# Kernel optimization log

Measured on AMD Instinct MI355X. Metric: run time of the kernel, lower is better.

The kernel has to match this reference:

```python
import jax, jax.numpy as jnp
import numpy as np

N_NODES = 50000
N_EDGES = 1_000_000
N_HYPER = 1024
F_IN = 128
F_EDGE = 64


def setup_inputs() -> dict:
    key = jax.random.key(0)
    ks = jax.random.split(key, 20)
    s = 0.05
    return {
        "x": jax.random.normal(ks[0], (N_NODES, F_IN), jnp.float32),
        "edge_index": jax.random.randint(ks[1], (2, N_EDGES), 0, N_NODES, dtype=jnp.int64),
        "edge_weight": jax.random.uniform(ks[2], (N_EDGES,), jnp.float32),
        "edge_features": jax.random.normal(ks[3], (N_HYPER, F_EDGE), jnp.float32),
        "adj_e": jax.random.uniform(ks[4], (N_HYPER, N_HYPER), jnp.float32) / N_HYPER,
        "T": jax.random.uniform(ks[5], (N_NODES, N_HYPER), jnp.float32) / N_HYPER,
        # HypergraphConvLayer 1: 128 -> 64
        "W1": jax.random.normal(ks[6], (F_IN, 64), jnp.float32) * s,
        "b1": jnp.zeros((64,), jnp.float32),
        # HypergraphConvLayer 2: 64 -> 32
        "W2": jax.random.normal(ks[7], (64, 32), jnp.float32) * s,
        "b2": jnp.zeros((32,), jnp.float32),
        # GraphConvolution (CensNet-style): node 32->32, edge 64->32
        "Wn": jax.random.normal(ks[8], (32, 32), jnp.float32) * s,
        "We": jax.random.normal(ks[9], (F_EDGE, 32), jnp.float32) * s,
        "bg": jnp.zeros((32,), jnp.float32),
        # class_classifier: Linear(32,32) -> ReLU -> Linear(32,2) -> Softmax
        "Wc1": jax.random.normal(ks[10], (32, 32), jnp.float32) * s,
        "bc1": jnp.zeros((32,), jnp.float32),
        "Wc2": jax.random.normal(ks[11], (32, 2), jnp.float32) * s,
        "bc2": jnp.zeros((2,), jnp.float32),
    }


def _hconv(h, W, b, src, dst, edge_weight, num_nodes):
    # linear projection then edge-weighted scatter-add: out[dst] += w * h[src]
    h = h @ W + b
    msg = h[src] * edge_weight[:, None]          # [E, d]
    return jax.ops.segment_sum(msg, dst, num_segments=num_nodes)


def reference(x, edge_index, edge_weight, edge_features, adj_e, T,
              W1, b1, W2, b2, Wn, We, bg, Wc1, bc1, Wc2, bc2):
    n = x.shape[0]
    src, dst = edge_index[0], edge_index[1]

    h = jax.nn.relu(_hconv(x, W1, b1, src, dst, edge_weight, n))   # [N,64]
    h = jax.nn.relu(_hconv(h, W2, b2, src, dst, edge_weight, n))   # [N,32]

    # aggregate_node_features: node_features[dst] += h[src]; / num_edges
    num_edges = edge_index.shape[1]
    node_features = jax.ops.segment_sum(h[src], dst, num_segments=n) / num_edges

    # edge_conv: node linear + incidence-weighted hyperedge convolution
    edge_h = adj_e @ (edge_features @ We)                           # [NE,32]
    shared = jax.nn.relu(node_features @ Wn + T @ edge_h + bg)      # [N,32]

    # class_classifier
    c = jax.nn.relu(shared @ Wc1 + bc1)
    logits = c @ Wc2 + bc2
    return jax.nn.softmax(logits, axis=1)                           # [N,2]
```

## Files before the change

kernel.cpp:

```cpp
#include <hip/hip_runtime.h>
#include <hip/hip_bf16.h>

template<int COLS, int K, int RPBT>
__global__ __launch_bounds__(256) void gemm_k(
    const float* __restrict__ X, const float* __restrict__ W,
    const float* __restrict__ bias, float* __restrict__ out,
    int nrows, float scale, int relu_in)
{
    constexpr int CPT = COLS / 8;
    constexpr int KT  = 32;
    constexpr int NKT = K / KT;
    constexpr int RT  = RPBT / 32;

    __shared__ float sx[RPBT * 36];
    __shared__ float sWT[COLS * 33];

    const int tid = threadIdx.x;
    const int cg  = tid & 7;
    const int rg  = tid >> 3;
    const int r0  = blockIdx.x * RPBT;

    float acc[RT][CPT];
    #pragma unroll
    for (int r = 0; r < RT; ++r)
        #pragma unroll
        for (int c = 0; c < CPT; ++c) acc[r][c] = 0.f;

    for (int kt = 0; kt < NKT; ++kt) {
        #pragma unroll
        for (int j = 0; j < RT; ++j) {
            int i  = tid + j * 256;
            int r  = i >> 3;
            int k4 = i & 7;
            int gr = r0 + r; if (gr >= nrows) gr = nrows - 1;
            float4 v = *(const float4*)&X[(size_t)gr * K + kt * KT + k4 * 4];
            if (relu_in) {
                v.x = fmaxf(v.x, 0.f); v.y = fmaxf(v.y, 0.f);
                v.z = fmaxf(v.z, 0.f); v.w = fmaxf(v.w, 0.f);
            }
            if (scale != 1.f) { v.x *= scale; v.y *= scale; v.z *= scale; v.w *= scale; }
            *(float4*)&sx[r * 36 + k4 * 4] = v;
        }
        for (int i = tid; i < COLS * KT; i += 256) {
            int kl = i / COLS, c = i % COLS;
            sWT[c * 33 + kl] = W[(size_t)(kt * KT + kl) * COLS + c];
        }
        __syncthreads();

        #pragma unroll
        for (int k4 = 0; k4 < 8; ++k4) {
            float4 a[RT];
            #pragma unroll
            for (int r = 0; r < RT; ++r)
                a[r] = *(const float4*)&sx[(r * 32 + rg) * 36 + k4 * 4];
            #pragma unroll
            for (int cc = 0; cc < CPT; ++cc) {
                int c = cg * CPT + cc;
                float w0 = sWT[c * 33 + k4 * 4 + 0];
                float w1 = sWT[c * 33 + k4 * 4 + 1];
                float w2 = sWT[c * 33 + k4 * 4 + 2];
                float w3 = sWT[c * 33 + k4 * 4 + 3];
                #pragma unroll
                for (int r = 0; r < RT; ++r)
                    acc[r][cc] += a[r].x * w0 + a[r].y * w1 + a[r].z * w2 + a[r].w * w3;
            }
        }
        __syncthreads();
    }

    #pragma unroll
    for (int r = 0; r < RT; ++r) {
        int row = r0 + r * 32 + rg;
        if (row < nrows) {
            #pragma unroll
            for (int cc4 = 0; cc4 < CPT / 4; ++cc4) {
                int c = cg * CPT + cc4 * 4;
                float4 o;
                o.x = acc[r][cc4 * 4 + 0] + (bias ? bias[c + 0] : 0.f);
                o.y = acc[r][cc4 * 4 + 1] + (bias ? bias[c + 1] : 0.f);
                o.z = acc[r][cc4 * 4 + 2] + (bias ? bias[c + 2] : 0.f);
                o.w = acc[r][cc4 * 4 + 3] + (bias ? bias[c + 3] : 0.f);
                *(float4*)&out[(size_t)row * COLS + c] = o;
            }
        }
    }
}

__global__ __launch_bounds__(256, 4) void tgemm2_k(
    const float* __restrict__ T, const float* __restrict__ eh,
    float* __restrict__ par, int nrows)
{
    __shared__ float seh[256 * 32];
    const int tid = threadIdx.x;
    const int ks  = blockIdx.y * 256;

    #pragma unroll
    for (int j = 0; j < 8; ++j) {
        int i = tid + j * 256;
        *(float4*)&seh[i * 4] = *(const float4*)&eh[(size_t)ks * 32 + (size_t)i * 4];
    }
    __syncthreads();

    int row = blockIdx.x * 256 + tid;
    int r   = row < nrows ? row : nrows - 1;
    const float* Tp = T + (size_t)r * 1024 + ks;

    float acc[32];
    #pragma unroll
    for (int c = 0; c < 32; ++c) acc[c] = 0.f;

    float4 t[8];
    #pragma unroll
    for (int q = 0; q < 8; ++q) t[q] = *(const float4*)&Tp[q * 4];

    for (int kc = 0; kc < 8; ++kc) {
        float4 tn[8];
        if (kc < 7) {
            #pragma unroll
            for (int q = 0; q < 8; ++q)
                tn[q] = *(const float4*)&Tp[(kc + 1) * 32 + q * 4];
        }
        #pragma unroll
        for (int q = 0; q < 8; ++q) {
            #pragma unroll
            for (int j = 0; j < 4; ++j) {
                float a = (j == 0) ? t[q].x : (j == 1) ? t[q].y : (j == 2) ? t[q].z : t[q].w;
                int k = kc * 32 + q * 4 + j;
                #pragma unroll
                for (int c4 = 0; c4 < 8; ++c4) {
                    float4 w = *(const float4*)&seh[k * 32 + c4 * 4];
                    acc[c4 * 4 + 0] += a * w.x;
                    acc[c4 * 4 + 1] += a * w.y;
                    acc[c4 * 4 + 2] += a * w.z;
                    acc[c4 * 4 + 3] += a * w.w;
                }
            }
        }
        #pragma unroll
        for (int q = 0; q < 8; ++q) t[q] = tn[q];
    }

    if (row < nrows) {
        float* p = par + (size_t)blockIdx.y * nrows * 32 + (size_t)row * 32;
        #pragma unroll
        for (int c4 = 0; c4 < 8; ++c4)
            *(float4*)&p[c4 * 4] = make_float4(acc[c4 * 4 + 0], acc[c4 * 4 + 1],
                                               acc[c4 * 4 + 2], acc[c4 * 4 + 3]);
    }
}

__global__ __launch_bounds__(256) void classify_k(
    const float* __restrict__ par, const float* __restrict__ nfw,
    const float* __restrict__ bg, const float* __restrict__ Wc1,
    const float* __restrict__ bc1, const float* __restrict__ Wc2,
    const float* __restrict__ bc2, float* __restrict__ out, int nrows)
{
    __shared__ float sWc1T[1024];
    __shared__ float sWc2[64];
    __shared__ float sb[66];

    int tid = threadIdx.x;
    for (int i = tid; i < 1024; i += 256)
        sWc1T[(i & 31) * 32 + (i >> 5)] = Wc1[i];
    if (tid < 64) sWc2[tid] = Wc2[tid];
    if (tid < 32)      sb[tid] = bc1[tid];
    else if (tid < 64) sb[tid] = bg[tid - 32];
    else if (tid < 66) sb[tid] = bc2[tid - 64];
    __syncthreads();

    int row = blockIdx.x * 256 + tid;
    if (row >= nrows) return;

    size_t stride = (size_t)nrows * 32;
    float4 sh4[8];
    #pragma unroll
    for (int i4 = 0; i4 < 8; ++i4) {
        const float* base = par + (size_t)row * 32 + i4 * 4;
        float4 v0 = *(const float4*)(base);
        float4 v1 = *(const float4*)(base + stride);
        float4 v2 = *(const float4*)(base + 2 * stride);
        float4 v3 = *(const float4*)(base + 3 * stride);
        float4 nf = *(const float4*)&nfw[(size_t)row * 32 + i4 * 4];
        float4 o;
        o.x = fmaxf(v0.x + v1.x + v2.x + v3.x + nf.x + sb[32 + i4 * 4 + 0], 0.f);
        o.y = fmaxf(v0.y + v1.y + v2.y + v3.y + nf.y + sb[32 + i4 * 4 + 1], 0.f);
        o.z = fmaxf(v0.z + v1.z + v2.z + v3.z + nf.z + sb[32 + i4 * 4 + 2], 0.f);
        o.w = fmaxf(v0.w + v1.w + v2.w + v3.w + nf.w + sb[32 + i4 * 4 + 3], 0.f);
        sh4[i4] = o;
    }

    float l0 = sb[64], l1 = sb[65];
    #pragma unroll
    for (int jj = 0; jj < 32; ++jj) {
        float s = sb[jj];
        #pragma unroll
        for (int i4 = 0; i4 < 8; ++i4) {
            float4 w4 = *(const float4*)&sWc1T[jj * 32 + i4 * 4];
            s += sh4[i4].x * w4.x + sh4[i4].y * w4.y
               + sh4[i4].z * w4.z + sh4[i4].w * w4.w;
        }
        s = fmaxf(s, 0.f);
        l0 += s * sWc2[jj * 2 + 0];
        l1 += s * sWc2[jj * 2 + 1];
    }
    float p0 = 1.f / (1.f + expf(l1 - l0));
    float p1 = 1.f / (1.f + expf(l0 - l1));
    *(float2*)&out[(size_t)row * 2] = make_float2(p0, p1);
}

__global__ void hist_k(const int* __restrict__ dst, int* __restrict__ deg, int E)
{
    int e = blockIdx.x * 256 + threadIdx.x;
    if (e < E) atomicAdd(&deg[dst[e]], 1);
}

__global__ void scan1_k(const int* __restrict__ deg, int* __restrict__ bsum, int N)
{
    __shared__ int s[256];
    int t = threadIdx.x, i = blockIdx.x * 256 + t;
    s[t] = (i < N) ? deg[i] : 0;
    __syncthreads();
    for (int off = 128; off > 0; off >>= 1) {
        if (t < off) s[t] += s[t + off];
        __syncthreads();
    }
    if (t == 0) bsum[blockIdx.x] = s[0];
}

__global__ void scan2_k(const int* __restrict__ bsum, int* __restrict__ boff,
                        int NB, int* __restrict__ rsN)
{
    __shared__ int s[256];
    int t = threadIdx.x;
    int v = (t < NB) ? bsum[t] : 0;
    s[t] = v;
    __syncthreads();
    for (int off = 1; off < 256; off <<= 1) {
        int u = (t >= off) ? s[t - off] : 0;
        __syncthreads();
        s[t] += u;
        __syncthreads();
    }
    if (t < NB) boff[t] = s[t] - v;
    if (t == NB - 1) *rsN = s[t];
}

__global__ void scan3_k(const int* __restrict__ deg, const int* __restrict__ boff,
                        int* __restrict__ rs, int* __restrict__ cur, int N)
{
    __shared__ int s[256];
    int t = threadIdx.x, i = blockIdx.x * 256 + t;
    int v = (i < N) ? deg[i] : 0;
    s[t] = v;
    __syncthreads();
    for (int off = 1; off < 256; off <<= 1) {
        int u = (t >= off) ? s[t - off] : 0;
        __syncthreads();
        s[t] += u;
        __syncthreads();
    }
    if (i < N) {
        int ex = boff[blockIdx.x] + s[t] - v;
        rs[i] = ex;
        cur[i] = ex;
    }
}

__global__ void fill_k(const int* __restrict__ src, const int* __restrict__ dst,
                       const float* __restrict__ ew, int* __restrict__ cur,
                       int2* __restrict__ epk, int E)
{
    int e = blockIdx.x * 256 + threadIdx.x;
    if (e < E) {
        int pos = atomicAdd(&cur[dst[e]], 1);
        epk[pos] = make_int2(src[e], __float_as_int(ew[e]));
    }
}

__global__ __launch_bounds__(256) void gather64w_k(
    const float* __restrict__ hp, const int2* __restrict__ epk,
    const int* __restrict__ rs, float* __restrict__ outv, int N)
{
    int wid  = (blockIdx.x * 256 + threadIdx.x) >> 6;
    if (wid >= N) return;
    int lane = threadIdx.x & 63;
    int e4   = lane >> 4;
    int ch   = lane & 15;
    int j0 = rs[wid], j1 = rs[wid + 1];

    float4 acc = make_float4(0.f, 0.f, 0.f, 0.f);
    for (int j = j0 + e4; j < j1; j += 4) {
        int2 e = epk[j];
        float w = __int_as_float(e.y);
        float4 v = *(const float4*)&hp[(size_t)e.x * 64 + ch * 4];
        acc.x += v.x * w; acc.y += v.y * w;
        acc.z += v.z * w; acc.w += v.w * w;
    }
    #pragma unroll
    for (int off = 16; off < 64; off <<= 1) {
        acc.x += __shfl_xor(acc.x, off);
        acc.y += __shfl_xor(acc.y, off);
        acc.z += __shfl_xor(acc.z, off);
        acc.w += __shfl_xor(acc.w, off);
    }
    if (e4 == 0)
        *(float4*)&outv[(size_t)wid * 64 + ch * 4] = acc;
}

template<bool WEIGHTED, bool RELU>
__global__ __launch_bounds__(256) void gather32w_k(
    const float* __restrict__ hp, const int2* __restrict__ epk,
    const int* __restrict__ rs, float* __restrict__ outv, int N)
{
    int wid  = (blockIdx.x * 256 + threadIdx.x) >> 6;
    if (wid >= N) return;
    int lane = threadIdx.x & 63;
    int e8   = lane >> 3;
    int ch   = lane & 7;
    int j0 = rs[wid], j1 = rs[wid + 1];

    float4 acc = make_float4(0.f, 0.f, 0.f, 0.f);
    for (int j = j0 + e8; j < j1; j += 8) {
        int2 e = epk[j];
        float w = WEIGHTED ? __int_as_float(e.y) : 1.f;
        float4 v = *(const float4*)&hp[(size_t)e.x * 32 + ch * 4];
        if (RELU) {
            v.x = fmaxf(v.x, 0.f); v.y = fmaxf(v.y, 0.f);
            v.z = fmaxf(v.z, 0.f); v.w = fmaxf(v.w, 0.f);
        }
        acc.x += v.x * w; acc.y += v.y * w;
        acc.z += v.z * w; acc.w += v.w * w;
    }
    #pragma unroll
    for (int off = 8; off < 64; off <<= 1) {
        acc.x += __shfl_xor(acc.x, off);
        acc.y += __shfl_xor(acc.y, off);
        acc.z += __shfl_xor(acc.z, off);
        acc.w += __shfl_xor(acc.w, off);
    }
    if (e8 == 0)
        *(float4*)&outv[(size_t)wid * 32 + ch * 4] = acc;
}

__global__ void efwe_k(const float* __restrict__ ef, const float* __restrict__ We,
                       float* __restrict__ tmp)
{
    int idx = blockIdx.x * 256 + threadIdx.x;
    int row = idx >> 5, c = idx & 31;
    float s = 0.f;
    #pragma unroll
    for (int k = 0; k < 64; ++k)
        s += ef[row * 64 + k] * We[k * 32 + c];
    tmp[row * 32 + c] = s;
}

__global__ void adjmm_k(const float* __restrict__ adj, const float* __restrict__ tmp,
                        float* __restrict__ edge_h)
{
    int kq     = blockIdx.x & 3;
    int rowblk = blockIdx.x >> 2;
    int r = rowblk * 8 + (threadIdx.x >> 5);
    int c = threadIdx.x & 31;
    float s = 0.f;
    int k0 = kq * 256;
    #pragma unroll 8
    for (int k = k0; k < k0 + 256; ++k)
        s += adj[r * 1024 + k] * tmp[k * 32 + c];
    atomicAdd(&edge_h[r * 32 + c], s);
}

extern "C" void kernel_launch(void* const* d_in, const int* in_sizes, int n_in,
                              void* d_out, int out_size, void* d_ws, size_t ws_size,
                              hipStream_t stream)
{
    const float* x   = (const float*)d_in[0];
    const int*   ei  = (const int*)  d_in[1];
    const float* ew  = (const float*)d_in[2];
    const float* ef  = (const float*)d_in[3];
    const float* adj = (const float*)d_in[4];
    const float* T   = (const float*)d_in[5];
    const float* W1  = (const float*)d_in[6];
    const float* b1  = (const float*)d_in[7];
    const float* W2  = (const float*)d_in[8];
    const float* b2  = (const float*)d_in[9];
    const float* Wn  = (const float*)d_in[10];
    const float* We  = (const float*)d_in[11];
    const float* bg  = (const float*)d_in[12];
    const float* Wc1 = (const float*)d_in[13];
    const float* bc1 = (const float*)d_in[14];
    const float* Wc2 = (const float*)d_in[15];
    const float* bc2 = (const float*)d_in[16];
    float* out = (float*)d_out;

    const int N = in_sizes[0] / 128;
    const int E = in_sizes[1] / 2;
    const int* srcIdx = ei;
    const int* dstIdx = ei + E;

    float* ws = (float*)d_ws;
    size_t o = 0;
    float* h1acc  = ws + o; o += (size_t)N * 64;
    float* h2acc  = ws + o; o += (size_t)N * 32;
    float* nfacc  = ws + o; o += (size_t)N * 32;
    float* edge_h = ws + o; o += 1024 * 32;
    float* tmp    = ws + o; o += 1024 * 32;
    float* nfw    = ws + o; o += (size_t)N * 32;
    float* par    = ws + o; o += (size_t)N * 128;
    float* h1p    = par;
    float* h2p    = par + (size_t)N * 64;
    int2*  epk    = (int2*)(ws + o);  o += (size_t)E * 2;
    int*   deg    = (int*)(ws + o);   o += N;
    int*   rs     = (int*)(ws + o);   o += N + 1;
    int*   cur    = (int*)(ws + o);   o += N + 1;
    int*   bsum   = (int*)(ws + o);   o += 256;
    int*   boff   = (int*)(ws + o);   o += 256;

    const int NB  = (N + 255) / 256;
    const int NBG = (N + 63) / 64;
    const int NBW = (N * 64 + 255) / 256;

    (void)hipMemsetAsync(deg, 0, (size_t)N * sizeof(int), stream);
    (void)hipMemsetAsync(edge_h, 0, 1024 * 32 * sizeof(float), stream);

    gemm_k<64, 128, 64><<<NBG, 256, 0, stream>>>(x, W1, b1, h1p, N, 1.f, 0);

    hist_k<<<(E + 255) / 256, 256, 0, stream>>>(dstIdx, deg, E);
    scan1_k<<<NB, 256, 0, stream>>>(deg, bsum, N);
    scan2_k<<<1, 256, 0, stream>>>(bsum, boff, NB, rs + N);
    scan3_k<<<NB, 256, 0, stream>>>(deg, boff, rs, cur, N);
    fill_k<<<(E + 255) / 256, 256, 0, stream>>>(srcIdx, dstIdx, ew, cur, epk, E);

    gather64w_k<<<NBW, 256, 0, stream>>>(h1p, epk, rs, h1acc, N);

    gemm_k<32, 64, 64><<<NBG, 256, 0, stream>>>(h1acc, W2, b2, h2p, N, 1.f, 1);

    gather32w_k<true, false><<<NBW, 256, 0, stream>>>(h2p, epk, rs, h2acc, N);

    gather32w_k<false, true><<<NBW, 256, 0, stream>>>(h2acc, epk, rs, nfacc, N);

    efwe_k<<<128, 256, 0, stream>>>(ef, We, tmp);
    adjmm_k<<<512, 256, 0, stream>>>(adj, tmp, edge_h);

    gemm_k<32, 32, 64><<<NBG, 256, 0, stream>>>(nfacc, Wn, nullptr, nfw, N, 1.f / (float)E, 0);

    tgemm2_k<<<dim3(NB, 4), 256, 0, stream>>>(T, edge_h, par, N);

    classify_k<<<NB, 256, 0, stream>>>(par, nfw, bg, Wc1, bc1, Wc2, bc2, out, N);
}
```

Measured before the change: 702.8 us.

## Store gathered node features in fp16 and fuse Wn projection into classifier

The projected node features that the three edge-gather passes read at random are now stored as fp16 instead of fp32, which halves the bytes fetched per edge. The ReLU is moved into the writer of the second gather, so the third gather reads already-rectified fp16 values. The separate Wn GEMM is folded into the classifier kernel, removing one launch and one N×32 intermediate round-trip through memory. In exchange, fp16 storage of intermediates adds rounding error and carries overflow risk in the final accumulations.

```diff
diff --git a/kernel.cpp b/kernel.cpp
--- a/kernel.cpp
+++ b/kernel.cpp
@@ -1,10 +1,10 @@
 #include <hip/hip_runtime.h>
-#include <hip/hip_bf16.h>
-
-template<int COLS, int K, int RPBT>
+#include <hip/hip_fp16.h>
+
+template<int COLS, int K, int RPBT, int OUTH>
 __global__ __launch_bounds__(256) void gemm_k(
     const float* __restrict__ X, const float* __restrict__ W,
-    const float* __restrict__ bias, float* __restrict__ out,
+    const float* __restrict__ bias, void* __restrict__ outp,
     int nrows, float scale, int relu_in)
 {
     constexpr int CPT = COLS / 8;
@@ -80,7 +80,16 @@
                 o.y = acc[r][cc4 * 4 + 1] + (bias ? bias[c + 1] : 0.f);
                 o.z = acc[r][cc4 * 4 + 2] + (bias ? bias[c + 2] : 0.f);
                 o.w = acc[r][cc4 * 4 + 3] + (bias ? bias[c + 3] : 0.f);
-                *(float4*)&out[(size_t)row * COLS + c] = o;
+                if constexpr (OUTH) {
+                    __half2 h0 = __floats2half2_rn(o.x, o.y);
+                    __half2 h1 = __floats2half2_rn(o.z, o.w);
+                    uint2 u;
+                    u.x = *(unsigned int*)&h0;
+                    u.y = *(unsigned int*)&h1;
+                    *(uint2*)&((__half*)outp)[(size_t)row * COLS + c] = u;
+                } else {
+                    *(float4*)&((float*)outp)[(size_t)row * COLS + c] = o;
+                }
             }
         }
     }
@@ -149,19 +158,23 @@
     }
 }
 
-__global__ __launch_bounds__(256) void classify_k(
-    const float* __restrict__ par, const float* __restrict__ nfw,
-    const float* __restrict__ bg, const float* __restrict__ Wc1,
-    const float* __restrict__ bc1, const float* __restrict__ Wc2,
-    const float* __restrict__ bc2, float* __restrict__ out, int nrows)
-{
+__global__ __launch_bounds__(256) void classify2_k(
+    const float* __restrict__ par, const float* __restrict__ nfacc,
+    const float* __restrict__ Wn, const float* __restrict__ bg,
+    const float* __restrict__ Wc1, const float* __restrict__ bc1,
+    const float* __restrict__ Wc2, const float* __restrict__ bc2,
+    float* __restrict__ out, int nrows, float invE)
+{
+    __shared__ float sWn[1024];
     __shared__ float sWc1T[1024];
     __shared__ float sWc2[64];
     __shared__ float sb[66];
 
     int tid = threadIdx.x;
-    for (int i = tid; i < 1024; i += 256)
+    for (int i = tid; i < 1024; i += 256) {
+        sWn[i] = Wn[i];
         sWc1T[(i & 31) * 32 + (i >> 5)] = Wc1[i];
+    }
     if (tid < 64) sWc2[tid] = Wc2[tid];
     if (tid < 32)      sb[tid] = bc1[tid];
     else if (tid < 64) sb[tid] = bg[tid - 32];
@@ -171,8 +184,31 @@
     int row = blockIdx.x * 256 + tid;
     if (row >= nrows) return;
 
+    float nf[32];
+    #pragma unroll
+    for (int i4 = 0; i4 < 8; ++i4) {
+        float4 v = *(const float4*)&nfacc[(size_t)row * 32 + i4 * 4];
+        nf[i4 * 4 + 0] = v.x * invE; nf[i4 * 4 + 1] = v.y * invE;
+        nf[i4 * 4 + 2] = v.z * invE; nf[i4 * 4 + 3] = v.w * invE;
+    }
+
+    float acc[32];
+    #pragma unroll
+    for (int c = 0; c < 32; ++c) acc[c] = sb[32 + c];
+    #pragma unroll
+    for (int k = 0; k < 32; ++k) {
+        float a = nf[k];
+        #pragma unroll
+        for (int c4 = 0; c4 < 8; ++c4) {
+            float4 w = *(const float4*)&sWn[k * 32 + c4 * 4];
+            acc[c4 * 4 + 0] += a * w.x;
+            acc[c4 * 4 + 1] += a * w.y;
+            acc[c4 * 4 + 2] += a * w.z;
+            acc[c4 * 4 + 3] += a * w.w;
+        }
+    }
+
     size_t stride = (size_t)nrows * 32;
-    float4 sh4[8];
     #pragma unroll
     for (int i4 = 0; i4 < 8; ++i4) {
         const float* base = par + (size_t)row * 32 + i4 * 4;
@@ -180,13 +216,10 @@
         float4 v1 = *(const float4*)(base + stride);
         float4 v2 = *(const float4*)(base + 2 * stride);
         float4 v3 = *(const float4*)(base + 3 * stride);
-        float4 nf = *(const float4*)&nfw[(size_t)row * 32 + i4 * 4];
-        float4 o;
-        o.x = fmaxf(v0.x + v1.x + v2.x + v3.x + nf.x + sb[32 + i4 * 4 + 0], 0.f);
-        o.y = fmaxf(v0.y + v1.y + v2.y + v3.y + nf.y + sb[32 + i4 * 4 + 1], 0.f);
-        o.z = fmaxf(v0.z + v1.z + v2.z + v3.z + nf.z + sb[32 + i4 * 4 + 2], 0.f);
-        o.w = fmaxf(v0.w + v1.w + v2.w + v3.w + nf.w + sb[32 + i4 * 4 + 3], 0.f);
-        sh4[i4] = o;
+        acc[i4 * 4 + 0] = fmaxf(acc[i4 * 4 + 0] + v0.x + v1.x + v2.x + v3.x, 0.f);
+        acc[i4 * 4 + 1] = fmaxf(acc[i4 * 4 + 1] + v0.y + v1.y + v2.y + v3.y, 0.f);
+        acc[i4 * 4 + 2] = fmaxf(acc[i4 * 4 + 2] + v0.z + v1.z + v2.z + v3.z, 0.f);
+        acc[i4 * 4 + 3] = fmaxf(acc[i4 * 4 + 3] + v0.w + v1.w + v2.w + v3.w, 0.f);
     }
 
     float l0 = sb[64], l1 = sb[65];
@@ -194,10 +227,10 @@
     for (int jj = 0; jj < 32; ++jj) {
         float s = sb[jj];
         #pragma unroll
-        for (int i4 = 0; i4 < 8; ++i4) {
-            float4 w4 = *(const float4*)&sWc1T[jj * 32 + i4 * 4];
-            s += sh4[i4].x * w4.x + sh4[i4].y * w4.y
-               + sh4[i4].z * w4.z + sh4[i4].w * w4.w;
+        for (int k4 = 0; k4 < 8; ++k4) {
+            float4 w4 = *(const float4*)&sWc1T[jj * 32 + k4 * 4];
+            s += acc[k4 * 4 + 0] * w4.x + acc[k4 * 4 + 1] * w4.y
+               + acc[k4 * 4 + 2] * w4.z + acc[k4 * 4 + 3] * w4.w;
         }
         s = fmaxf(s, 0.f);
         l0 += s * sWc2[jj * 2 + 0];
@@ -277,8 +310,8 @@
     }
 }
 
-__global__ __launch_bounds__(256) void gather64w_k(
-    const float* __restrict__ hp, const int2* __restrict__ epk,
+__global__ __launch_bounds__(256) void gather64h_k(
+    const __half* __restrict__ hp, const int2* __restrict__ epk,
     const int* __restrict__ rs, float* __restrict__ outv, int N)
 {
     int wid  = (blockIdx.x * 256 + threadIdx.x) >> 6;
@@ -292,9 +325,11 @@
     for (int j = j0 + e4; j < j1; j += 4) {
         int2 e = epk[j];
         float w = __int_as_float(e.y);
-        float4 v = *(const float4*)&hp[(size_t)e.x * 64 + ch * 4];
-        acc.x += v.x * w; acc.y += v.y * w;
-        acc.z += v.z * w; acc.w += v.w * w;
+        uint2 u = *(const uint2*)&hp[(size_t)e.x * 64 + ch * 4];
+        float2 a = __half22float2(*(__half2*)&u.x);
+        float2 b = __half22float2(*(__half2*)&u.y);
+        acc.x += a.x * w; acc.y += a.y * w;
+        acc.z += b.x * w; acc.w += b.y * w;
     }
     #pragma unroll
     for (int off = 16; off < 64; off <<= 1) {
@@ -307,10 +342,9 @@
         *(float4*)&outv[(size_t)wid * 64 + ch * 4] = acc;
 }
 
-template<bool WEIGHTED, bool RELU>
-__global__ __launch_bounds__(256) void gather32w_k(
-    const float* __restrict__ hp, const int2* __restrict__ epk,
-    const int* __restrict__ rs, float* __restrict__ outv, int N)
+__global__ __launch_bounds__(256) void gather32h_wr_k(
+    const __half* __restrict__ hp, const int2* __restrict__ epk,
+    const int* __restrict__ rs, __half* __restrict__ outh, int N)
 {
     int wid  = (blockIdx.x * 256 + threadIdx.x) >> 6;
     if (wid >= N) return;
@@ -322,14 +356,49 @@
     float4 acc = make_float4(0.f, 0.f, 0.f, 0.f);
     for (int j = j0 + e8; j < j1; j += 8) {
         int2 e = epk[j];
-        float w = WEIGHTED ? __int_as_float(e.y) : 1.f;
-        float4 v = *(const float4*)&hp[(size_t)e.x * 32 + ch * 4];
-        if (RELU) {
-            v.x = fmaxf(v.x, 0.f); v.y = fmaxf(v.y, 0.f);
-            v.z = fmaxf(v.z, 0.f); v.w = fmaxf(v.w, 0.f);
-        }
-        acc.x += v.x * w; acc.y += v.y * w;
-        acc.z += v.z * w; acc.w += v.w * w;
+        float w = __int_as_float(e.y);
+        uint2 u = *(const uint2*)&hp[(size_t)e.x * 32 + ch * 4];
+        float2 a = __half22float2(*(__half2*)&u.x);
+        float2 b = __half22float2(*(__half2*)&u.y);
+        acc.x += a.x * w; acc.y += a.y * w;
+        acc.z += b.x * w; acc.w += b.y * w;
+    }
+    #pragma unroll
+    for (int off = 8; off < 64; off <<= 1) {
+        acc.x += __shfl_xor(acc.x, off);
+        acc.y += __shfl_xor(acc.y, off);
+        acc.z += __shfl_xor(acc.z, off);
+        acc.w += __shfl_xor(acc.w, off);
+    }
+    if (e8 == 0) {
+        __half2 h0 = __floats2half2_rn(fmaxf(acc.x, 0.f), fmaxf(acc.y, 0.f));
+        __half2 h1 = __floats2half2_rn(fmaxf(acc.z, 0.f), fmaxf(acc.w, 0.f));
+        uint2 u;
+        u.x = *(unsigned int*)&h0;
+        u.y = *(unsigned int*)&h1;
+        *(uint2*)&outh[(size_t)wid * 32 + ch * 4] = u;
+    }
+}
+
+__global__ __launch_bounds__(256) void gather32h_uf_k(
+    const __half* __restrict__ hp, const int2* __restrict__ epk,
+    const int* __restrict__ rs, float* __restrict__ outv, int N)
+{
+    int wid  = (blockIdx.x * 256 + threadIdx.x) >> 6;
+    if (wid >= N) return;
+    int lane = threadIdx.x & 63;
+    int e8   = lane >> 3;
+    int ch   = lane & 7;
+    int j0 = rs[wid], j1 = rs[wid + 1];
+
+    float4 acc = make_float4(0.f, 0.f, 0.f, 0.f);
+    for (int j = j0 + e8; j < j1; j += 8) {
+        int2 e = epk[j];
+        uint2 u = *(const uint2*)&hp[(size_t)e.x * 32 + ch * 4];
+        float2 a = __half22float2(*(__half2*)&u.x);
+        float2 b = __half22float2(*(__half2*)&u.y);
+        acc.x += a.x; acc.y += a.y;
+        acc.z += b.x; acc.w += b.y;
     }
     #pragma unroll
     for (int off = 8; off < 64; off <<= 1) {
@@ -399,21 +468,20 @@
 
     float* ws = (float*)d_ws;
     size_t o = 0;
-    float* h1acc  = ws + o; o += (size_t)N * 64;
-    float* h2acc  = ws + o; o += (size_t)N * 32;
-    float* nfacc  = ws + o; o += (size_t)N * 32;
-    float* edge_h = ws + o; o += 1024 * 32;
-    float* tmp    = ws + o; o += 1024 * 32;
-    float* nfw    = ws + o; o += (size_t)N * 32;
-    float* par    = ws + o; o += (size_t)N * 128;
-    float* h1p    = par;
-    float* h2p    = par + (size_t)N * 64;
-    int2*  epk    = (int2*)(ws + o);  o += (size_t)E * 2;
-    int*   deg    = (int*)(ws + o);   o += N;
-    int*   rs     = (int*)(ws + o);   o += N + 1;
-    int*   cur    = (int*)(ws + o);   o += N + 1;
-    int*   bsum   = (int*)(ws + o);   o += 256;
-    int*   boff   = (int*)(ws + o);   o += 256;
+    float*  h1acc  = ws + o; o += (size_t)N * 64;
+    float*  nfacc  = ws + o; o += (size_t)N * 32;
+    float*  edge_h = ws + o; o += 1024 * 32;
+    float*  tmp    = ws + o; o += 1024 * 32;
+    float*  par    = ws + o; o += (size_t)N * 128;
+    __half* h1p_h  = (__half*)(ws + o); o += (size_t)N * 32;
+    __half* h2p_h  = (__half*)(ws + o); o += (size_t)N * 16;
+    __half* h2r_h  = (__half*)(ws + o); o += (size_t)N * 16;
+    int2*   epk    = (int2*)(ws + o);   o += (size_t)E * 2;
+    int*    deg    = (int*)(ws + o);    o += N;
+    int*    rs     = (int*)(ws + o);    o += N + 1;
+    int*    cur    = (int*)(ws + o);    o += N + 1;
+    int*    bsum   = (int*)(ws + o);    o += 256;
+    int*    boff   = (int*)(ws + o);    o += 256;
 
     const int NB  = (N + 255) / 256;
     const int NBG = (N + 63) / 64;
@@ -422,7 +490,7 @@
     (void)hipMemsetAsync(deg, 0, (size_t)N * sizeof(int), stream);
     (void)hipMemsetAsync(edge_h, 0, 1024 * 32 * sizeof(float), stream);
 
-    gemm_k<64, 128, 64><<<NBG, 256, 0, stream>>>(x, W1, b1, h1p, N, 1.f, 0);
+    gemm_k<64, 128, 64, 1><<<NBG, 256, 0, stream>>>(x, W1, b1, h1p_h, N, 1.f, 0);
 
     hist_k<<<(E + 255) / 256, 256, 0, stream>>>(dstIdx, deg, E);
     scan1_k<<<NB, 256, 0, stream>>>(deg, bsum, N);
@@ -430,20 +498,19 @@
     scan3_k<<<NB, 256, 0, stream>>>(deg, boff, rs, cur, N);
     fill_k<<<(E + 255) / 256, 256, 0, stream>>>(srcIdx, dstIdx, ew, cur, epk, E);
 
-    gather64w_k<<<NBW, 256, 0, stream>>>(h1p, epk, rs, h1acc, N);
-
-    gemm_k<32, 64, 64><<<NBG, 256, 0, stream>>>(h1acc, W2, b2, h2p, N, 1.f, 1);
-
-    gather32w_k<true, false><<<NBW, 256, 0, stream>>>(h2p, epk, rs, h2acc, N);
-
-    gather32w_k<false, true><<<NBW, 256, 0, stream>>>(h2acc, epk, rs, nfacc, N);
+    gather64h_k<<<NBW, 256, 0, stream>>>(h1p_h, epk, rs, h1acc, N);
+
+    gemm_k<32, 64, 64, 1><<<NBG, 256, 0, stream>>>(h1acc, W2, b2, h2p_h, N, 1.f, 1);
+
+    gather32h_wr_k<<<NBW, 256, 0, stream>>>(h2p_h, epk, rs, h2r_h, N);
+
+    gather32h_uf_k<<<NBW, 256, 0, stream>>>(h2r_h, epk, rs, nfacc, N);
 
     efwe_k<<<128, 256, 0, stream>>>(ef, We, tmp);
     adjmm_k<<<512, 256, 0, stream>>>(adj, tmp, edge_h);
 
-    gemm_k<32, 32, 64><<<NBG, 256, 0, stream>>>(nfacc, Wn, nullptr, nfw, N, 1.f / (float)E, 0);
-
     tgemm2_k<<<dim3(NB, 4), 256, 0, stream>>>(T, edge_h, par, N);
 
-    classify_k<<<NB, 256, 0, stream>>>(par, nfw, bg, Wc1, bc1, Wc2, bc2, out, N);
-}
+    classify2_k<<<NB, 256, 0, stream>>>(par, nfacc, Wn, bg, Wc1, bc1, Wc2, bc2,
+                                        out, N, 1.f / (float)E);
+}
```

After: 687.5 us. 1.02x faster.
